# Kernel tuning notes

Hardware: AMD Instinct MI355X
Metric: run time of the kernel (lower is better)

The kernel has to match this reference:

```python
import jax, jax.numpy as jnp
import numpy as np

B, N, D, H = 8, 2048, 512, 8  # batch, seq (incl. CLS), emb_dim, heads


def setup_inputs() -> dict:
    key = jax.random.key(0)
    kx, km, k1, k2, k3, k4 = jax.random.split(key, 6)
    x = jax.random.normal(kx, (B, N, D), dtype=jnp.float32)
    # mask covers the N-1 non-CLS tokens; forward pads a leading True for CLS
    mask = jax.random.bernoulli(km, p=0.9, shape=(B, N - 1))
    s = 0.02
    Wqkv = jax.random.normal(k1, (D, 3 * D), dtype=jnp.float32) * s
    bqkv = jax.random.normal(k2, (3 * D,), dtype=jnp.float32) * s
    Wout = jax.random.normal(k3, (D, D), dtype=jnp.float32) * s
    bout = jax.random.normal(k4, (D,), dtype=jnp.float32) * s
    return {"x": x, "mask": mask, "Wqkv": Wqkv, "bqkv": bqkv,
            "Wout": Wout, "bout": bout, "num_heads": H}


def reference(x, mask, Wqkv, bqkv, Wout, bout, num_heads):
    b, n, d = x.shape
    h = num_heads
    dh = d // h
    scale = d ** (-0.5)  # NOTE: module scales by emb_dim^-0.5, not head_dim^-0.5

    qkv = x @ Wqkv + bqkv                      # [b, n, 3d]
    q, k, v = jnp.split(qkv, 3, axis=-1)
    def to_heads(t):
        return t.reshape(b, n, h, dh).transpose(0, 2, 1, 3)  # [b, h, n, dh]
    q, k, v = map(to_heads, (q, k, v))

    scores = jnp.einsum('bhqd,bhkd->bhqk', q, k) * scale     # [b, h, n, n]

    # pad leading True for CLS token, then outer-product pair mask
    m = jnp.pad(mask, ((0, 0), (1, 0)), constant_values=True)  # [b, n]
    pair = m[:, None, :, None] & m[:, None, None, :]           # [b, 1, n, n]
    neg = jnp.asarray(-1e9, dtype=scores.dtype)  # finite stand-in for -inf (avoids NaN rows)
    scores = jnp.where(pair, scores, neg)

    attn = jax.nn.softmax(scores, axis=-1)
    out = jnp.einsum('bhqk,bhkd->bhqd', attn, v)               # [b, h, n, dh]
    out = out.transpose(0, 2, 1, 3).reshape(b, n, d)
    return out @ Wout + bout
```

## Files before the change

kernel.cpp:

```cpp
#include <hip/hip_runtime.h>
#include <math.h>

#define BB  8
#define SEQ 2048
#define EMB 512
#define NH  8
#define DH  64
#define NBH (BB * NH)
#define MROWS (BB * SEQ)
#define QKV_ELEMS ((size_t)NBH * SEQ * DH)
#define MASK_ELEMS (BB * (SEQ - 1))
#define QSCALE 0.06375871307545f

typedef __attribute__((ext_vector_type(8)))  short short8;
typedef __attribute__((ext_vector_type(4)))  float float4e;
typedef __attribute__((ext_vector_type(16))) float float16e;
typedef __attribute__((ext_vector_type(4)))  unsigned int uint4e;
typedef unsigned short ushort_t;

static __device__ inline unsigned short f2bf(float f) {
    unsigned int u = __float_as_uint(f);
    unsigned int r = (u + 0x7fffu + ((u >> 16) & 1u)) >> 16;
    return (unsigned short)r;
}

static __device__ inline void gl_lds16(const unsigned short* g, unsigned short* l) {
    __builtin_amdgcn_global_load_lds(
        (const __attribute__((address_space(1))) void*)g,
        (__attribute__((address_space(3))) void*)l, 16, 0, 0);
}

#define PREP_CONV   8192
#define PREP_MASK   (PREP_CONV + 64)
#define PREP_WQ     (PREP_MASK + (1536 / 32) * (EMB / 32))
#define PREP_TOTAL  (PREP_WQ + (EMB / 32) * (EMB / 32))

__global__ __launch_bounds__(256) void prep(const float* __restrict__ x,
                                            const void* __restrict__ mraw,
                                            const float* __restrict__ Wqkv,
                                            const float* __restrict__ Wout,
                                            ushort_t* __restrict__ xb,
                                            float* __restrict__ pmf,
                                            ushort_t* __restrict__ wqt,
                                            ushort_t* __restrict__ wot) {
    __shared__ float T[32][33];
    __shared__ int flag;
    const int bid = blockIdx.x;
    const int tid = threadIdx.x;

    if (bid < PREP_CONV) {
        const size_t i = ((size_t)bid * 256 + tid) * 4;
        float4 v = *(const float4*)&x[i];
        ushort4 o;
        o.x = f2bf(v.x); o.y = f2bf(v.y); o.z = f2bf(v.z); o.w = f2bf(v.w);
        *(ushort4*)&xb[i] = o;
    } else if (bid < PREP_MASK) {
        if (tid == 0) flag = 0;
        __syncthreads();
        const unsigned int* mi = (const unsigned int*)mraw;
        int local = 0;
        for (int i = tid; i < MASK_ELEMS / 4; i += 256) {
            if (mi[i] > 1u) local = 1;
        }
        if (local) flag = 1;
        __syncthreads();
        const int isbyte = flag;
        const unsigned char* mb = (const unsigned char*)mraw;
        const int* m32 = (const int*)mraw;
        const int i = (bid - PREP_CONV) * 256 + tid;
        const int b = i >> 11, n = i & (SEQ - 1);
        int v;
        if (n == 0) v = 1;
        else {
            const int src = b * (SEQ - 1) + n - 1;
            v = isbyte ? (int)mb[src] : (m32[src] != 0 ? 1 : 0);
        }
        pmf[i] = v ? 1.0f : 0.0f;
    } else {
        const float* src;
        ushort_t* dst;
        int N, idx;
        if (bid < PREP_WQ) {
            src = Wqkv; dst = wqt; N = 1536; idx = bid - PREP_MASK;
        } else {
            src = Wout; dst = wot; N = EMB; idx = bid - PREP_WQ;
        }
        const int nb = N / 32;
        const int n0 = (idx % nb) * 32;
        const int k0 = (idx / nb) * 32;
        {
            const int r = tid >> 3, c4 = (tid & 7) * 4;
            *(float4*)&T[r][c4] = *(const float4*)&src[(size_t)(k0 + r) * N + n0 + c4];
        }
        __syncthreads();
        const int n = tid >> 3, k4 = (tid & 7) * 4;
        ushort4 hv;
        hv.x = f2bf(T[k4 + 0][n]);
        hv.y = f2bf(T[k4 + 1][n]);
        hv.z = f2bf(T[k4 + 2][n]);
        hv.w = f2bf(T[k4 + 3][n]);
        *(ushort4*)&dst[(size_t)(n0 + n) * EMB + k0 + k4] = hv;
    }
}

__global__ __launch_bounds__(256) void qkv_mfma(const ushort_t* __restrict__ xb,
                                                const ushort_t* __restrict__ wt,
                                                const float* __restrict__ bias,
                                                ushort_t* __restrict__ qb,
                                                ushort_t* __restrict__ kb,
                                                ushort_t* __restrict__ vt) {
    __shared__ __align__(16) ushort_t As[128 * 32];
    __shared__ __align__(16) ushort_t Bs[128 * 32];
    const int tid  = threadIdx.x;
    const int w    = tid >> 6;
    const int lane = tid & 63;
    const int l16  = lane & 15;
    const int quad = lane >> 4;
    const int wq   = w >> 1;
    const int wn   = w & 1;
    const int row0 = blockIdx.y * 128;
    const int col0 = blockIdx.x * 128;

    float4e acc[4][4];
    #pragma unroll
    for (int i = 0; i < 4; ++i)
        #pragma unroll
        for (int j = 0; j < 4; ++j) acc[i][j] = (float4e){0.f, 0.f, 0.f, 0.f};

    const int srow = tid >> 2;
    const int csrc = (tid & 3) ^ (srow & 3);

    for (int k0 = 0; k0 < EMB; k0 += 32) {
        #pragma unroll
        for (int s = 0; s < 2; ++s) {
            const int row = s * 64 + srow;
            gl_lds16(xb + (size_t)(row0 + row) * EMB + k0 + csrc * 8,
                     As + s * 2048 + w * 512);
            gl_lds16(wt + (size_t)(col0 + row) * EMB + k0 + csrc * 8,
                     Bs + s * 2048 + w * 512);
        }
        __syncthreads();
        short8 af[4], bf[4];
        #pragma unroll
        for (int mt = 0; mt < 4; ++mt) {
            const int rm = wq * 64 + mt * 16 + l16;
            af[mt] = *(const short8*)(As + rm * 32 + ((quad ^ (rm & 3)) * 8));
        }
        #pragma unroll
        for (int nt = 0; nt < 4; ++nt) {
            const int rn = wn * 64 + nt * 16 + l16;
            bf[nt] = *(const short8*)(Bs + rn * 32 + ((quad ^ (rn & 3)) * 8));
        }
        #pragma unroll
        for (int mt = 0; mt < 4; ++mt)
            #pragma unroll
            for (int nt = 0; nt < 4; ++nt)
                acc[mt][nt] = __builtin_amdgcn_mfma_f32_16x16x32_bf16(af[mt], bf[nt], acc[mt][nt], 0, 0, 0);
        __syncthreads();
    }

    #pragma unroll
    for (int nt = 0; nt < 4; ++nt) {
        const int cb    = col0 + wn * 64 + nt * 16;
        const int which = cb >> 9;
        const int h     = (cb >> 6) & 7;
        const int dcol  = (cb & 63) + l16;
        const float bz  = bias[cb + l16];
        if (which == 2) {
            #pragma unroll
            for (int mt = 0; mt < 4; ++mt) {
                const int rg = row0 + wq * 64 + mt * 16 + quad * 4;
                const int b = rg >> 11, n = rg & (SEQ - 1);
                ushort4 ov;
                ov.x = f2bf(acc[mt][nt][0] + bz);
                ov.y = f2bf(acc[mt][nt][1] + bz);
                ov.z = f2bf(acc[mt][nt][2] + bz);
                ov.w = f2bf(acc[mt][nt][3] + bz);
                *(ushort4*)&vt[((size_t)(b * NH + h) * DH + dcol) * SEQ + n] = ov;
            }
        } else {
            ushort_t* base = (which == 0) ? qb : kb;
            const float sc = (which == 0) ? QSCALE : 1.0f;
            #pragma unroll
            for (int mt = 0; mt < 4; ++mt) {
                #pragma unroll
                for (int i = 0; i < 4; ++i) {
                    const int rg = row0 + wq * 64 + mt * 16 + quad * 4 + i;
                    const int b = rg >> 11;
                    const int n = rg & (SEQ - 1);
                    base[((size_t)(b * NH + h) * SEQ + n) * DH + dcol] =
                        f2bf((acc[mt][nt][i] + bz) * sc);
                }
            }
        }
    }
}

__device__ inline void stage_tile(const ushort_t* kbh, const ushort_t* vbh, int kt,
                                  ushort_t* Kd, ushort_t* Vd,
                                  const int* crow, const int* csoff, int wbase) {
    #pragma unroll
    for (int j = 0; j < 4; ++j) {
        gl_lds16(kbh + (size_t)(kt * 64 + crow[j]) * DH + csoff[j],
                 Kd + (j * 128 + wbase) * 8);
        gl_lds16(vbh + (size_t)crow[j] * SEQ + kt * 64 + csoff[j],
                 Vd + (j * 128 + wbase) * 8);
    }
}

__global__ __launch_bounds__(128, 2) void attn_mfma(const ushort_t* __restrict__ qb,
                                                    const ushort_t* __restrict__ kb,
                                                    const ushort_t* __restrict__ vt,
                                                    const float* __restrict__ pmf,
                                                    ushort_t* __restrict__ ab) {
    __shared__ __align__(16) ushort_t Ks[2][64 * 64];
    __shared__ __align__(16) ushort_t Vts[2][64 * 64];
    __shared__ float lw[2][64];

    const int tid = threadIdx.x;
    const int w   = tid >> 6;
    const int lane = tid & 63;
    const int l5  = lane & 31;
    const int h   = lane >> 5;
    const int qt  = blockIdx.x & 15;
    const int bh  = blockIdx.x >> 4;
    const int b   = bh >> 3;
    const int hh  = bh & 7;
    const int q0  = qt * 128 + w * 64;

    const ushort_t* qbh = qb + (size_t)bh * SEQ * DH;
    short8 qf[2][4];
    #pragma unroll
    for (int t = 0; t < 2; ++t)
        #pragma unroll
        for (int kc = 0; kc < 4; ++kc)
            qf[t][kc] = *(const short8*)(qbh + (size_t)(q0 + t * 32 + l5) * DH + kc * 16 + h * 8);

    float mq[2], fnq[2];
    #pragma unroll
    for (int t = 0; t < 2; ++t) {
        mq[t]  = pmf[b * SEQ + q0 + t * 32 + l5];
        fnq[t] = 1.0f - mq[t];
    }

    int crow[4], csoff[4];
    #pragma unroll
    for (int j = 0; j < 4; ++j) {
        const int c = j * 128 + tid;
        crow[j]  = c >> 3;
        csoff[j] = ((c & 7) ^ (crow[j] & 7)) * 8;
    }
    const int wbase = w * 64;
    const ushort_t* kbh = kb + (size_t)bh * SEQ * DH;
    const ushort_t* vbh = vt + (size_t)bh * DH * SEQ;
    const float*    mrow = pmf + b * SEQ;

    float16e o[2][2];
    #pragma unroll
    for (int t = 0; t < 2; ++t)
        #pragma unroll
        for (int d = 0; d < 2; ++d) o[t][d] = (float16e)0.0f;
    float l_i[2] = {0.f, 0.f};

    stage_tile(kbh, vbh, 0, Ks[0], Vts[0], crow, csoff, wbase);

    for (int kt = 0; kt < 32; ++kt) {
        __syncthreads();
        const int cur = kt & 1;
        if (kt < 31)
            stage_tile(kbh, vbh, kt + 1, Ks[cur ^ 1], Vts[cur ^ 1], crow, csoff, wbase);

        #pragma unroll
        for (int s = 0; s < 2; ++s) {
            const int krow = s * 32 + l5;
            short8 kf[4];
            #pragma unroll
            for (int kc = 0; kc < 4; ++kc)
                kf[kc] = *(const short8*)(Ks[cur] + krow * 64 + (((kc * 2 + h) ^ (krow & 7)) * 8));
            float16e st[2];
            st[0] = (float16e)0.0f;
            st[1] = (float16e)0.0f;
            #pragma unroll
            for (int kc = 0; kc < 4; ++kc) {
                st[0] = __builtin_amdgcn_mfma_f32_32x32x16_bf16(kf[kc], qf[0][kc], st[0], 0, 0, 0);
                st[1] = __builtin_amdgcn_mfma_f32_32x32x16_bf16(kf[kc], qf[1][kc], st[1], 0, 0, 0);
            }

            float4e mk4[4];
            #pragma unroll
            for (int g2 = 0; g2 < 4; ++g2)
                mk4[g2] = *(const float4e*)(mrow + kt * 64 + s * 32 + g2 * 8 + h * 4);

            short8 af[2][2];
            #pragma unroll
            for (int t = 0; t < 2; ++t) {
                unsigned int a[8];
                float lacc = 0.f;
                #pragma unroll
                for (int j = 0; j < 8; ++j) {
                    const float mk0 = mk4[j >> 1][(2 * j) & 3];
                    const float mk1 = mk4[j >> 1][(2 * j + 1) & 3];
                    const float p0 = fmaf(__builtin_amdgcn_exp2f(st[t][2 * j]) * mk0, mq[t], fnq[t]);
                    const float p1 = fmaf(__builtin_amdgcn_exp2f(st[t][2 * j + 1]) * mk1, mq[t], fnq[t]);
                    lacc += p0 + p1;
                    a[j] = (__float_as_uint(p0) >> 16) | (__float_as_uint(p1) & 0xffff0000u);
                }
                l_i[t] += lacc;
                #pragma unroll
                for (int c = 0; c < 2; ++c) {
                    const unsigned int s0 = h ? a[4 * c]     : a[4 * c + 2];
                    const unsigned int s1 = h ? a[4 * c + 1] : a[4 * c + 3];
                    const unsigned int x0 = (unsigned int)__shfl_xor((int)s0, 32);
                    const unsigned int x1 = (unsigned int)__shfl_xor((int)s1, 32);
                    uint4e fv;
                    fv.x = h ? x0 : a[4 * c];
                    fv.y = h ? x1 : a[4 * c + 1];
                    fv.z = h ? a[4 * c + 2] : x0;
                    fv.w = h ? a[4 * c + 3] : x1;
                    af[t][c] = __builtin_bit_cast(short8, fv);
                }
            }

            #pragma unroll
            for (int c = 0; c < 2; ++c) {
                #pragma unroll
                for (int d = 0; d < 2; ++d) {
                    const int vrow = d * 32 + l5;
                    const short8 vf = *(const short8*)(Vts[cur] + vrow * 64 +
                                       (((s * 4 + c * 2 + h) ^ (vrow & 7)) * 8));
                    o[0][d] = __builtin_amdgcn_mfma_f32_32x32x16_bf16(af[0][c], vf, o[0][d], 0, 0, 0);
                    o[1][d] = __builtin_amdgcn_mfma_f32_32x32x16_bf16(af[1][c], vf, o[1][d], 0, 0, 0);
                }
            }
        }
    }

    #pragma unroll
    for (int t = 0; t < 2; ++t) {
        const float l = l_i[t] + __shfl_xor(l_i[t], 32);
        lw[w][t * 32 + l5] = l;
    }

    ushort_t* ob = ab + ((size_t)b * SEQ + q0) * EMB + hh * DH;
    #pragma unroll
    for (int t = 0; t < 2; ++t) {
        #pragma unroll
        for (int r = 0; r < 16; ++r) {
            const int ql = (r & 3) + 8 * (r >> 2) + 4 * h;
            const float inv = 1.0f / lw[w][t * 32 + ql];
            #pragma unroll
            for (int d = 0; d < 2; ++d)
                ob[(size_t)(t * 32 + ql) * EMB + d * 32 + l5] = f2bf(o[t][d][r] * inv);
        }
    }
}

__global__ __launch_bounds__(256) void out_mfma(const ushort_t* __restrict__ ab,
                                                const ushort_t* __restrict__ wot,
                                                const float* __restrict__ bias,
                                                float* __restrict__ out) {
    __shared__ __align__(16) ushort_t As[128 * 32];
    __shared__ __align__(16) ushort_t Bs[128 * 32];
    const int tid  = threadIdx.x;
    const int w    = tid >> 6;
    const int lane = tid & 63;
    const int l16  = lane & 15;
    const int quad = lane >> 4;
    const int wq   = w >> 1;
    const int wn   = w & 1;
    const int row0 = blockIdx.y * 128;
    const int col0 = blockIdx.x * 128;

    float4e acc[4][4];
    #pragma unroll
    for (int i = 0; i < 4; ++i)
        #pragma unroll
        for (int j = 0; j < 4; ++j) acc[i][j] = (float4e){0.f, 0.f, 0.f, 0.f};

    const int srow = tid >> 2;
    const int csrc = (tid & 3) ^ (srow & 3);

    for (int k0 = 0; k0 < EMB; k0 += 32) {
        #pragma unroll
        for (int s = 0; s < 2; ++s) {
            const int row = s * 64 + srow;
            gl_lds16(ab + (size_t)(row0 + row) * EMB + k0 + csrc * 8,
                     As + s * 2048 + w * 512);
            gl_lds16(wot + (size_t)(col0 + row) * EMB + k0 + csrc * 8,
                     Bs + s * 2048 + w * 512);
        }
        __syncthreads();
        short8 af[4], bf[4];
        #pragma unroll
        for (int mt = 0; mt < 4; ++mt) {
            const int rm = wq * 64 + mt * 16 + l16;
            af[mt] = *(const short8*)(As + rm * 32 + ((quad ^ (rm & 3)) * 8));
        }
        #pragma unroll
        for (int nt = 0; nt < 4; ++nt) {
            const int rn = wn * 64 + nt * 16 + l16;
            bf[nt] = *(const short8*)(Bs + rn * 32 + ((quad ^ (rn & 3)) * 8));
        }
        #pragma unroll
        for (int mt = 0; mt < 4; ++mt)
            #pragma unroll
            for (int nt = 0; nt < 4; ++nt)
                acc[mt][nt] = __builtin_amdgcn_mfma_f32_16x16x32_bf16(af[mt], bf[nt], acc[mt][nt], 0, 0, 0);
        __syncthreads();
    }

    #pragma unroll
    for (int nt = 0; nt < 4; ++nt) {
        const int col_g = col0 + wn * 64 + nt * 16 + l16;
        const float bz = bias[col_g];
        #pragma unroll
        for (int mt = 0; mt < 4; ++mt) {
            #pragma unroll
            for (int i = 0; i < 4; ++i) {
                const int row_g = row0 + wq * 64 + mt * 16 + quad * 4 + i;
                out[(size_t)row_g * EMB + col_g] = acc[mt][nt][i] + bz;
            }
        }
    }
}

extern "C" void kernel_launch(void* const* d_in, const int* in_sizes, int n_in,
                              void* d_out, int out_size, void* d_ws, size_t ws_size,
                              hipStream_t stream) {
    const float* x    = (const float*)d_in[0];
    const void*  mask = d_in[1];
    const float* Wqkv = (const float*)d_in[2];
    const float* bqkv = (const float*)d_in[3];
    const float* Wout = (const float*)d_in[4];
    const float* bout = (const float*)d_in[5];
    float* out = (float*)d_out;

    ushort_t* xb  = (ushort_t*)d_ws;
    ushort_t* wqt = xb + (size_t)MROWS * EMB;
    ushort_t* wot = wqt + (size_t)1536 * EMB;
    ushort_t* qb  = wot + (size_t)EMB * EMB;
    ushort_t* kb  = qb + QKV_ELEMS;
    ushort_t* vt  = kb + QKV_ELEMS;
    ushort_t* ab  = vt + QKV_ELEMS;
    float*    pmf = (float*)(ab + (size_t)MROWS * EMB);

    prep<<<dim3(PREP_TOTAL), 256, 0, stream>>>(x, mask, Wqkv, Wout, xb, pmf, wqt, wot);
    qkv_mfma<<<dim3(1536 / 128, MROWS / 128), 256, 0, stream>>>(xb, wqt, bqkv, qb, kb, vt);
    attn_mfma<<<dim3(NBH * (SEQ / 128)), 128, 0, stream>>>(qb, kb, vt, pmf, ab);
    out_mfma<<<dim3(EMB / 128, MROWS / 128), 256, 0, stream>>>(ab, wot, bout, out);
}
```

Baseline: 257.7 us.

## Restructure attention to 4 waves of 32 queries with permlane swap and priorities

The attention kernel moves from 2 waves that each own 64 query rows to 4 waves that each own 32 query rows per 128-query block. This halves per-wave accumulator and register use, and the launch bound allows 4 blocks per CU instead of 2. It also precomputes mask*mq once per key chunk, replaces the select-and-shuffle exchange with permlane32_swap, wraps the MFMA sections in s_setprio, and remaps block IDs so each XCD processes contiguous heads. The tradeoff is that each wave now does less MFMA work per K/V tile load, which lowers reuse of the staged LDS tiles.

```diff
diff --git a/kernel.cpp b/kernel.cpp
--- a/kernel.cpp
+++ b/kernel.cpp
@@ -16,6 +16,7 @@
 typedef __attribute__((ext_vector_type(4)))  float float4e;
 typedef __attribute__((ext_vector_type(16))) float float16e;
 typedef __attribute__((ext_vector_type(4)))  unsigned int uint4e;
+typedef __attribute__((ext_vector_type(2)))  unsigned int uint2e;
 typedef unsigned short ushort_t;
 
 static __device__ inline unsigned short f2bf(float f) {
@@ -200,53 +201,49 @@
                                   ushort_t* Kd, ushort_t* Vd,
                                   const int* crow, const int* csoff, int wbase) {
     #pragma unroll
-    for (int j = 0; j < 4; ++j) {
+    for (int j = 0; j < 2; ++j) {
         gl_lds16(kbh + (size_t)(kt * 64 + crow[j]) * DH + csoff[j],
-                 Kd + (j * 128 + wbase) * 8);
+                 Kd + (j * 256 + wbase) * 8);
         gl_lds16(vbh + (size_t)crow[j] * SEQ + kt * 64 + csoff[j],
-                 Vd + (j * 128 + wbase) * 8);
-    }
-}
-
-__global__ __launch_bounds__(128, 2) void attn_mfma(const ushort_t* __restrict__ qb,
+                 Vd + (j * 256 + wbase) * 8);
+    }
+}
+
+__global__ __launch_bounds__(256, 4) void attn_mfma(const ushort_t* __restrict__ qb,
                                                     const ushort_t* __restrict__ kb,
                                                     const ushort_t* __restrict__ vt,
                                                     const float* __restrict__ pmf,
                                                     ushort_t* __restrict__ ab) {
     __shared__ __align__(16) ushort_t Ks[2][64 * 64];
     __shared__ __align__(16) ushort_t Vts[2][64 * 64];
-    __shared__ float lw[2][64];
+    __shared__ float lw[4][32];
 
     const int tid = threadIdx.x;
     const int w   = tid >> 6;
     const int lane = tid & 63;
     const int l5  = lane & 31;
     const int h   = lane >> 5;
-    const int qt  = blockIdx.x & 15;
-    const int bh  = blockIdx.x >> 4;
+    const int bid = blockIdx.x;
+    const int ord = bid >> 3;
+    const int bh  = (bid & 7) * 8 + (ord >> 4);
+    const int qt  = ord & 15;
     const int b   = bh >> 3;
     const int hh  = bh & 7;
-    const int q0  = qt * 128 + w * 64;
+    const int q0  = qt * 128 + w * 32;
 
     const ushort_t* qbh = qb + (size_t)bh * SEQ * DH;
-    short8 qf[2][4];
-    #pragma unroll
-    for (int t = 0; t < 2; ++t)
-        #pragma unroll
-        for (int kc = 0; kc < 4; ++kc)
-            qf[t][kc] = *(const short8*)(qbh + (size_t)(q0 + t * 32 + l5) * DH + kc * 16 + h * 8);
-
-    float mq[2], fnq[2];
-    #pragma unroll
-    for (int t = 0; t < 2; ++t) {
-        mq[t]  = pmf[b * SEQ + q0 + t * 32 + l5];
-        fnq[t] = 1.0f - mq[t];
-    }
-
-    int crow[4], csoff[4];
-    #pragma unroll
-    for (int j = 0; j < 4; ++j) {
-        const int c = j * 128 + tid;
+    short8 qf[4];
+    #pragma unroll
+    for (int kc = 0; kc < 4; ++kc)
+        qf[kc] = *(const short8*)(qbh + (size_t)(q0 + l5) * DH + kc * 16 + h * 8);
+
+    const float mq  = pmf[b * SEQ + q0 + l5];
+    const float fnq = 1.0f - mq;
+
+    int crow[2], csoff[2];
+    #pragma unroll
+    for (int j = 0; j < 2; ++j) {
+        const int c = j * 256 + tid;
         crow[j]  = c >> 3;
         csoff[j] = ((c & 7) ^ (crow[j] & 7)) * 8;
     }
@@ -255,12 +252,10 @@
     const ushort_t* vbh = vt + (size_t)bh * DH * SEQ;
     const float*    mrow = pmf + b * SEQ;
 
-    float16e o[2][2];
-    #pragma unroll
-    for (int t = 0; t < 2; ++t)
-        #pragma unroll
-        for (int d = 0; d < 2; ++d) o[t][d] = (float16e)0.0f;
-    float l_i[2] = {0.f, 0.f};
+    float16e o[2];
+    o[0] = (float16e)0.0f;
+    o[1] = (float16e)0.0f;
+    float l_i = 0.f;
 
     stage_tile(kbh, vbh, 0, Ks[0], Vts[0], crow, csoff, wbase);
 
@@ -272,55 +267,52 @@
 
         #pragma unroll
         for (int s = 0; s < 2; ++s) {
+            float4e m4[4];
+            #pragma unroll
+            for (int g2 = 0; g2 < 4; ++g2) {
+                const float4e raw = *(const float4e*)(mrow + kt * 64 + s * 32 + g2 * 8 + h * 4);
+                m4[g2] = raw * mq;
+            }
+
             const int krow = s * 32 + l5;
             short8 kf[4];
             #pragma unroll
             for (int kc = 0; kc < 4; ++kc)
                 kf[kc] = *(const short8*)(Ks[cur] + krow * 64 + (((kc * 2 + h) ^ (krow & 7)) * 8));
-            float16e st[2];
-            st[0] = (float16e)0.0f;
-            st[1] = (float16e)0.0f;
-            #pragma unroll
-            for (int kc = 0; kc < 4; ++kc) {
-                st[0] = __builtin_amdgcn_mfma_f32_32x32x16_bf16(kf[kc], qf[0][kc], st[0], 0, 0, 0);
-                st[1] = __builtin_amdgcn_mfma_f32_32x32x16_bf16(kf[kc], qf[1][kc], st[1], 0, 0, 0);
-            }
-
-            float4e mk4[4];
-            #pragma unroll
-            for (int g2 = 0; g2 < 4; ++g2)
-                mk4[g2] = *(const float4e*)(mrow + kt * 64 + s * 32 + g2 * 8 + h * 4);
-
-            short8 af[2][2];
-            #pragma unroll
-            for (int t = 0; t < 2; ++t) {
-                unsigned int a[8];
-                float lacc = 0.f;
-                #pragma unroll
-                for (int j = 0; j < 8; ++j) {
-                    const float mk0 = mk4[j >> 1][(2 * j) & 3];
-                    const float mk1 = mk4[j >> 1][(2 * j + 1) & 3];
-                    const float p0 = fmaf(__builtin_amdgcn_exp2f(st[t][2 * j]) * mk0, mq[t], fnq[t]);
-                    const float p1 = fmaf(__builtin_amdgcn_exp2f(st[t][2 * j + 1]) * mk1, mq[t], fnq[t]);
-                    lacc += p0 + p1;
-                    a[j] = (__float_as_uint(p0) >> 16) | (__float_as_uint(p1) & 0xffff0000u);
-                }
-                l_i[t] += lacc;
-                #pragma unroll
-                for (int c = 0; c < 2; ++c) {
-                    const unsigned int s0 = h ? a[4 * c]     : a[4 * c + 2];
-                    const unsigned int s1 = h ? a[4 * c + 1] : a[4 * c + 3];
-                    const unsigned int x0 = (unsigned int)__shfl_xor((int)s0, 32);
-                    const unsigned int x1 = (unsigned int)__shfl_xor((int)s1, 32);
-                    uint4e fv;
-                    fv.x = h ? x0 : a[4 * c];
-                    fv.y = h ? x1 : a[4 * c + 1];
-                    fv.z = h ? a[4 * c + 2] : x0;
-                    fv.w = h ? a[4 * c + 3] : x1;
-                    af[t][c] = __builtin_bit_cast(short8, fv);
-                }
-            }
-
+            float16e st = (float16e)0.0f;
+            __builtin_amdgcn_s_setprio(1);
+            #pragma unroll
+            for (int kc = 0; kc < 4; ++kc)
+                st = __builtin_amdgcn_mfma_f32_32x32x16_bf16(kf[kc], qf[kc], st, 0, 0, 0);
+            __builtin_amdgcn_s_setprio(0);
+
+            unsigned int a[8];
+            float lacc = 0.f;
+            #pragma unroll
+            for (int j = 0; j < 8; ++j) {
+                const float mk0 = m4[j >> 1][(2 * j) & 3];
+                const float mk1 = m4[j >> 1][(2 * j + 1) & 3];
+                const float p0 = fmaf(__builtin_amdgcn_exp2f(st[2 * j]),     mk0, fnq);
+                const float p1 = fmaf(__builtin_amdgcn_exp2f(st[2 * j + 1]), mk1, fnq);
+                lacc += p0 + p1;
+                a[j] = (__float_as_uint(p0) >> 16) | (__float_as_uint(p1) & 0xffff0000u);
+            }
+            l_i += lacc;
+
+            short8 af[2];
+            #pragma unroll
+            for (int c = 0; c < 2; ++c) {
+                const uint2e r02 = __builtin_amdgcn_permlane32_swap(a[4 * c],     a[4 * c + 2], false, false);
+                const uint2e r13 = __builtin_amdgcn_permlane32_swap(a[4 * c + 1], a[4 * c + 3], false, false);
+                uint4e fv;
+                fv.x = r02[0];
+                fv.y = r13[0];
+                fv.z = r02[1];
+                fv.w = r13[1];
+                af[c] = __builtin_bit_cast(short8, fv);
+            }
+
+            __builtin_amdgcn_s_setprio(1);
             #pragma unroll
             for (int c = 0; c < 2; ++c) {
                 #pragma unroll
@@ -328,30 +320,26 @@
                     const int vrow = d * 32 + l5;
                     const short8 vf = *(const short8*)(Vts[cur] + vrow * 64 +
                                        (((s * 4 + c * 2 + h) ^ (vrow & 7)) * 8));
-                    o[0][d] = __builtin_amdgcn_mfma_f32_32x32x16_bf16(af[0][c], vf, o[0][d], 0, 0, 0);
-                    o[1][d] = __builtin_amdgcn_mfma_f32_32x32x16_bf16(af[1][c], vf, o[1][d], 0, 0, 0);
+                    o[d] = __builtin_amdgcn_mfma_f32_32x32x16_bf16(af[c], vf, o[d], 0, 0, 0);
                 }
             }
-        }
-    }
-
-    #pragma unroll
-    for (int t = 0; t < 2; ++t) {
-        const float l = l_i[t] + __shfl_xor(l_i[t], 32);
-        lw[w][t * 32 + l5] = l;
+            __builtin_amdgcn_s_setprio(0);
+        }
+    }
+
+    {
+        const float l = l_i + __shfl_xor(l_i, 32);
+        lw[w][l5] = l;
     }
 
     ushort_t* ob = ab + ((size_t)b * SEQ + q0) * EMB + hh * DH;
     #pragma unroll
-    for (int t = 0; t < 2; ++t) {
-        #pragma unroll
-        for (int r = 0; r < 16; ++r) {
-            const int ql = (r & 3) + 8 * (r >> 2) + 4 * h;
-            const float inv = 1.0f / lw[w][t * 32 + ql];
-            #pragma unroll
-            for (int d = 0; d < 2; ++d)
-                ob[(size_t)(t * 32 + ql) * EMB + d * 32 + l5] = f2bf(o[t][d][r] * inv);
-        }
+    for (int r = 0; r < 16; ++r) {
+        const int ql = (r & 3) + 8 * (r >> 2) + 4 * h;
+        const float inv = 1.0f / lw[w][ql];
+        #pragma unroll
+        for (int d = 0; d < 2; ++d)
+            ob[(size_t)ql * EMB + d * 32 + l5] = f2bf(o[d][r] * inv);
     }
 }
 
@@ -446,6 +434,6 @@
 
     prep<<<dim3(PREP_TOTAL), 256, 0, stream>>>(x, mask, Wqkv, Wout, xb, pmf, wqt, wot);
     qkv_mfma<<<dim3(1536 / 128, MROWS / 128), 256, 0, stream>>>(xb, wqt, bqkv, qb, kb, vt);
-    attn_mfma<<<dim3(NBH * (SEQ / 128)), 128, 0, stream>>>(qb, kb, vt, pmf, ab);
+    attn_mfma<<<dim3(NBH * (SEQ / 128)), 256, 0, stream>>>(qb, kb, vt, pmf, ab);
     out_mfma<<<dim3(EMB / 128, MROWS / 128), 256, 0, stream>>>(ab, wot, bout, out);
 }
```

New measurement: 258.1 us. About the same (+0.1%).

## Fold key mask into MFMA accumulator init and use permlane32_swap

Applied to the files above, without the earlier changes.

Replaces the per-element mask multiply/FMA after exp2 with an additive bias (0 or -1e9) preloaded into the score accumulator, so masking rides on the MFMA. Masked query rows get zeroed Q fragments and a zero bias row, so every key scores equally, which reproduces the uniform-softmax behaviour. It also swaps the shfl_xor-based half-wave exchange for permlane32_swap, adds s_setprio around the MFMA blocks, and remaps block indices to interleave heads across the grid. It costs extra prep outputs (bias arrays) and global loads of the bias per tile, in exchange for fewer VALU ops in the softmax inner loop.

```diff
diff --git a/kernel.cpp b/kernel.cpp
--- a/kernel.cpp
+++ b/kernel.cpp
@@ -16,6 +16,7 @@
 typedef __attribute__((ext_vector_type(4)))  float float4e;
 typedef __attribute__((ext_vector_type(16))) float float16e;
 typedef __attribute__((ext_vector_type(4)))  unsigned int uint4e;
+typedef __attribute__((ext_vector_type(2)))  unsigned int uint2e;
 typedef unsigned short ushort_t;
 
 static __device__ inline unsigned short f2bf(float f) {
@@ -41,6 +42,8 @@
                                             const float* __restrict__ Wout,
                                             ushort_t* __restrict__ xb,
                                             float* __restrict__ pmf,
+                                            float* __restrict__ mkl,
+                                            float* __restrict__ zrow,
                                             ushort_t* __restrict__ wqt,
                                             ushort_t* __restrict__ wot) {
     __shared__ float T[32][33];
@@ -76,6 +79,8 @@
             v = isbyte ? (int)mb[src] : (m32[src] != 0 ? 1 : 0);
         }
         pmf[i] = v ? 1.0f : 0.0f;
+        mkl[i] = v ? 0.0f : -1e9f;
+        if (i < SEQ) zrow[i] = 0.0f;
     } else {
         const float* src;
         ushort_t* dst;
@@ -212,6 +217,8 @@
                                                     const ushort_t* __restrict__ kb,
                                                     const ushort_t* __restrict__ vt,
                                                     const float* __restrict__ pmf,
+                                                    const float* __restrict__ mkl,
+                                                    const float* __restrict__ zrow,
                                                     ushort_t* __restrict__ ab) {
     __shared__ __align__(16) ushort_t Ks[2][64 * 64];
     __shared__ __align__(16) ushort_t Vts[2][64 * 64];
@@ -222,8 +229,10 @@
     const int lane = tid & 63;
     const int l5  = lane & 31;
     const int h   = lane >> 5;
-    const int qt  = blockIdx.x & 15;
-    const int bh  = blockIdx.x >> 4;
+    const int bid = blockIdx.x;
+    const int ord = bid >> 3;
+    const int bh  = (bid & 7) * 8 + (ord >> 4);
+    const int qt  = ord & 15;
     const int b   = bh >> 3;
     const int hh  = bh & 7;
     const int q0  = qt * 128 + w * 64;
@@ -236,11 +245,16 @@
         for (int kc = 0; kc < 4; ++kc)
             qf[t][kc] = *(const short8*)(qbh + (size_t)(q0 + t * 32 + l5) * DH + kc * 16 + h * 8);
 
-    float mq[2], fnq[2];
+    const float* crb[2];
     #pragma unroll
     for (int t = 0; t < 2; ++t) {
-        mq[t]  = pmf[b * SEQ + q0 + t * 32 + l5];
-        fnq[t] = 1.0f - mq[t];
+        const float mq = pmf[b * SEQ + q0 + t * 32 + l5];
+        if (mq == 0.0f) {
+            const short8 z8 = {0, 0, 0, 0, 0, 0, 0, 0};
+            #pragma unroll
+            for (int kc = 0; kc < 4; ++kc) qf[t][kc] = z8;
+        }
+        crb[t] = (mq != 0.0f) ? (mkl + b * SEQ) : zrow;
     }
 
     int crow[4], csoff[4];
@@ -253,7 +267,6 @@
     const int wbase = w * 64;
     const ushort_t* kbh = kb + (size_t)bh * SEQ * DH;
     const ushort_t* vbh = vt + (size_t)bh * DH * SEQ;
-    const float*    mrow = pmf + b * SEQ;
 
     float16e o[2][2];
     #pragma unroll
@@ -272,24 +285,30 @@
 
         #pragma unroll
         for (int s = 0; s < 2; ++s) {
+            float16e st[2];
+            #pragma unroll
+            for (int t = 0; t < 2; ++t) {
+                #pragma unroll
+                for (int g2 = 0; g2 < 4; ++g2) {
+                    const float4e c4 = *(const float4e*)(crb[t] + kt * 64 + s * 32 + g2 * 8 + h * 4);
+                    #pragma unroll
+                    for (int j = 0; j < 4; ++j)
+                        st[t][g2 * 4 + j] = c4[j];
+                }
+            }
+
             const int krow = s * 32 + l5;
             short8 kf[4];
             #pragma unroll
             for (int kc = 0; kc < 4; ++kc)
                 kf[kc] = *(const short8*)(Ks[cur] + krow * 64 + (((kc * 2 + h) ^ (krow & 7)) * 8));
-            float16e st[2];
-            st[0] = (float16e)0.0f;
-            st[1] = (float16e)0.0f;
+            __builtin_amdgcn_s_setprio(1);
             #pragma unroll
             for (int kc = 0; kc < 4; ++kc) {
                 st[0] = __builtin_amdgcn_mfma_f32_32x32x16_bf16(kf[kc], qf[0][kc], st[0], 0, 0, 0);
                 st[1] = __builtin_amdgcn_mfma_f32_32x32x16_bf16(kf[kc], qf[1][kc], st[1], 0, 0, 0);
             }
-
-            float4e mk4[4];
-            #pragma unroll
-            for (int g2 = 0; g2 < 4; ++g2)
-                mk4[g2] = *(const float4e*)(mrow + kt * 64 + s * 32 + g2 * 8 + h * 4);
+            __builtin_amdgcn_s_setprio(0);
 
             short8 af[2][2];
             #pragma unroll
@@ -298,29 +317,26 @@
                 float lacc = 0.f;
                 #pragma unroll
                 for (int j = 0; j < 8; ++j) {
-                    const float mk0 = mk4[j >> 1][(2 * j) & 3];
-                    const float mk1 = mk4[j >> 1][(2 * j + 1) & 3];
-                    const float p0 = fmaf(__builtin_amdgcn_exp2f(st[t][2 * j]) * mk0, mq[t], fnq[t]);
-                    const float p1 = fmaf(__builtin_amdgcn_exp2f(st[t][2 * j + 1]) * mk1, mq[t], fnq[t]);
+                    const float p0 = __builtin_amdgcn_exp2f(st[t][2 * j]);
+                    const float p1 = __builtin_amdgcn_exp2f(st[t][2 * j + 1]);
                     lacc += p0 + p1;
                     a[j] = (__float_as_uint(p0) >> 16) | (__float_as_uint(p1) & 0xffff0000u);
                 }
                 l_i[t] += lacc;
                 #pragma unroll
                 for (int c = 0; c < 2; ++c) {
-                    const unsigned int s0 = h ? a[4 * c]     : a[4 * c + 2];
-                    const unsigned int s1 = h ? a[4 * c + 1] : a[4 * c + 3];
-                    const unsigned int x0 = (unsigned int)__shfl_xor((int)s0, 32);
-                    const unsigned int x1 = (unsigned int)__shfl_xor((int)s1, 32);
+                    const uint2e r02 = __builtin_amdgcn_permlane32_swap(a[4 * c],     a[4 * c + 2], false, false);
+                    const uint2e r13 = __builtin_amdgcn_permlane32_swap(a[4 * c + 1], a[4 * c + 3], false, false);
                     uint4e fv;
-                    fv.x = h ? x0 : a[4 * c];
-                    fv.y = h ? x1 : a[4 * c + 1];
-                    fv.z = h ? a[4 * c + 2] : x0;
-                    fv.w = h ? a[4 * c + 3] : x1;
+                    fv.x = r02[0];
+                    fv.y = r13[0];
+                    fv.z = r02[1];
+                    fv.w = r13[1];
                     af[t][c] = __builtin_bit_cast(short8, fv);
                 }
             }
 
+            __builtin_amdgcn_s_setprio(1);
             #pragma unroll
             for (int c = 0; c < 2; ++c) {
                 #pragma unroll
@@ -332,6 +348,7 @@
                     o[1][d] = __builtin_amdgcn_mfma_f32_32x32x16_bf16(af[1][c], vf, o[1][d], 0, 0, 0);
                 }
             }
+            __builtin_amdgcn_s_setprio(0);
         }
     }
 
@@ -443,9 +460,11 @@
     ushort_t* vt  = kb + QKV_ELEMS;
     ushort_t* ab  = vt + QKV_ELEMS;
     float*    pmf = (float*)(ab + (size_t)MROWS * EMB);
-
-    prep<<<dim3(PREP_TOTAL), 256, 0, stream>>>(x, mask, Wqkv, Wout, xb, pmf, wqt, wot);
+    float*    mkl = pmf + (size_t)BB * SEQ;
+    float*    zrw = mkl + (size_t)BB * SEQ;
+
+    prep<<<dim3(PREP_TOTAL), 256, 0, stream>>>(x, mask, Wqkv, Wout, xb, pmf, mkl, zrw, wqt, wot);
     qkv_mfma<<<dim3(1536 / 128, MROWS / 128), 256, 0, stream>>>(xb, wqt, bqkv, qb, kb, vt);
-    attn_mfma<<<dim3(NBH * (SEQ / 128)), 128, 0, stream>>>(qb, kb, vt, pmf, ab);
+    attn_mfma<<<dim3(NBH * (SEQ / 128)), 128, 0, stream>>>(qb, kb, vt, pmf, mkl, zrw, ab);
     out_mfma<<<dim3(EMB / 128, MROWS / 128), 256, 0, stream>>>(ab, wot, bout, out);
 }
```

Measured after the change: 250.8 us. 2.7% less time.
